# Kernel tuning notes

Hardware: AMD Instinct MI355X
Metric: run time of the kernel (lower is better)

The kernel has to match this reference:

```python
import jax, jax.numpy as jnp
import numpy as np

N = 100000      # nodes
E = 800000      # edges (avg degree 8)
F = 5           # num_node_features
D = 128         # embed_dim
H = 4           # heads
HD = D // H     # per-head dim = 32
H1, H2 = 64, 128  # mlp hidden dims


def _mlp(x, W1, b1, W2, b2, W3, b3):
    h = jax.nn.relu(x @ W1 + b1)
    h = jax.nn.relu(h @ W2 + b2)
    return h @ W3 + b3


def setup_inputs() -> dict:
    key = jax.random.key(0)
    ks = jax.random.split(key, 24)
    g = lambda i, shape: (jax.random.normal(ks[i], shape, dtype=jnp.float32) * 0.05)
    z = lambda d: jnp.zeros((d,), dtype=jnp.float32)
    return {
        "x": jax.random.normal(ks[0], (N, F), dtype=jnp.float32),
        "edge_index": jax.random.randint(ks[1], (2, E), 0, N),
        # mlp_prep: F -> 64 -> 128 -> D
        "prep_W1": g(2, (F, H1)),  "prep_b1": z(H1),
        "prep_W2": g(3, (H1, H2)), "prep_b2": z(H2),
        "prep_W3": g(4, (H2, D)),  "prep_b3": z(D),
        # mlp_update: D -> 64 -> 128 -> D
        "upd_W1": g(5, (D, H1)),   "upd_b1": z(H1),
        "upd_W2": g(6, (H1, H2)),  "upd_b2": z(H2),
        "upd_W3": g(7, (H2, D)),   "upd_b3": z(D),
        # TransformerConv projections (heads=4, per-head 32, concat -> D)
        "q_W": g(8, (D, D)),  "q_b": z(D),
        "k_W": g(9, (D, D)),  "k_b": z(D),
        "v_W": g(10, (D, D)), "v_b": z(D),
        "skip_W": g(11, (D, D)), "skip_b": z(D),
    }


def _transformer_conv(x, edge_index, q_W, q_b, k_W, k_b, v_W, v_b, skip_W, skip_b):
    # PyG TransformerConv: messages flow src=edge_index[0] -> dst=edge_index[1]
    src, dst = edge_index[0], edge_index[1]
    q = (x @ q_W + q_b).reshape(N, H, HD)
    k = (x @ k_W + k_b).reshape(N, H, HD)
    v = (x @ v_W + v_b).reshape(N, H, HD)
    scale = 1.0 / np.sqrt(HD).astype(np.float32)
    # per-edge attention logits [E, H]
    score = jnp.einsum('ehd,ehd->eh', q[dst], k[src]) * scale
    # segment softmax over incoming edges of each destination node
    m = jax.ops.segment_max(score, dst, num_segments=N)          # [N, H]
    e = jnp.exp(score - m[dst])                                  # [E, H]
    denom = jax.ops.segment_sum(e, dst, num_segments=N)         # [N, H]
    alpha = e / denom[dst]                                       # [E, H]
    # scatter-aggregate weighted values
    agg = jax.ops.segment_sum(alpha[..., None] * v[src], dst, num_segments=N)  # [N, H, HD]
    return agg.reshape(N, H * HD) + (x @ skip_W + skip_b)


def reference(x, edge_index,
              prep_W1, prep_b1, prep_W2, prep_b2, prep_W3, prep_b3,
              upd_W1, upd_b1, upd_W2, upd_b2, upd_W3, upd_b3,
              q_W, q_b, k_W, k_b, v_W, v_b, skip_W, skip_b):
    h_init = _mlp(x, prep_W1, prep_b1, prep_W2, prep_b2, prep_W3, prep_b3)
    h = _transformer_conv(h_init, edge_index, q_W, q_b, k_W, k_b, v_W, v_b, skip_W, skip_b)
    return h + _mlp(h, upd_W1, upd_b1, upd_W2, upd_b2, upd_W3, upd_b3)
```

## Files before the change

### kernel.cpp

```cpp
#include <hip/hip_runtime.h>
#include <hip/hip_bf16.h>

#define N_  100000
#define F_  5
#define D_  128
#define H_  4
#define HD_ 32
#define E_  800000

typedef __attribute__((ext_vector_type(8))) short bf16x8;
typedef __attribute__((ext_vector_type(4))) float f32x4;

__device__ __forceinline__ unsigned short f2bf(float f) {
  unsigned u = __float_as_uint(f);
  u += 0x7FFF + ((u >> 16) & 1);
  return (unsigned short)(u >> 16);
}

__device__ __forceinline__ unsigned pk2(float a, float b) {
  __hip_bfloat162 h = __float22bfloat162_rn(make_float2(a, b));
  return *(unsigned*)&h;
}

__device__ __forceinline__ float2 bf2f2(unsigned u) {
  float2 r;
  r.x = __uint_as_float(u << 16);
  r.y = __uint_as_float(u & 0xffff0000u);
  return r;
}

__device__ __forceinline__ float rowsum8(float x) {
  x += __int_as_float(__builtin_amdgcn_update_dpp(0, __float_as_int(x), 0x0B1, 0xF, 0xF, false));
  x += __int_as_float(__builtin_amdgcn_update_dpp(0, __float_as_int(x), 0x04E, 0xF, 0xF, false));
  x += __int_as_float(__builtin_amdgcn_update_dpp(0, __float_as_int(x), 0x141, 0xF, 0xF, false));
  return x;
}

template<int K, int M>
__device__ __forceinline__ void wconv_one(const float* __restrict__ W,
                                          unsigned short* __restrict__ WT,
                                          int idx) {
  const int r = idx & 7;
  const int l = (idx >> 3) & 15;
  const int rest = idx >> 7;
  const int kq = rest % (K / 8);
  const int i  = rest / (K / 8);
  WT[idx] = f2bf(W[(kq * 8 + r) * M + i * 16 + l]);
}

#define WCONV_NB 480
#define SCAN_NB ((N_ + 255) / 256)

__global__ __launch_bounds__(256) void k_wconv_all(
    const float* __restrict__ w0, const float* __restrict__ w1,
    const float* __restrict__ w2, const float* __restrict__ w3,
    const float* __restrict__ w4, const float* __restrict__ w5,
    const float* __restrict__ w6, const float* __restrict__ w7,
    const float* __restrict__ w8, unsigned short* __restrict__ WT,
    int* __restrict__ deg)
{
  if (blockIdx.x >= WCONV_NB) {
    const int i = (blockIdx.x - WCONV_NB) * 256 + threadIdx.x;
    if (i < N_) deg[i] = 0;
    return;
  }
  const int idx = blockIdx.x * 256 + threadIdx.x;
  if (idx < 8192)        wconv_one<64, 128>(w0, WT,          idx);
  else if (idx < 24576)  wconv_one<128,128>(w1, WT + 8192,   idx - 8192);
  else if (idx < 40960)  wconv_one<128,128>(w2, WT + 24576,  idx - 24576);
  else if (idx < 57344)  wconv_one<128,128>(w3, WT + 40960,  idx - 40960);
  else if (idx < 73728)  wconv_one<128,128>(w4, WT + 57344,  idx - 57344);
  else if (idx < 90112)  wconv_one<128,128>(w5, WT + 73728,  idx - 73728);
  else if (idx < 98304)  wconv_one<128, 64>(w6, WT + 90112,  idx - 90112);
  else if (idx < 106496) wconv_one<64, 128>(w7, WT + 98304,  idx - 98304);
  else                   wconv_one<128,128>(w8, WT + 106496, idx - 106496);
}

template<int K, int M>
__device__ __forceinline__ void gemm_frag(const unsigned short* sX,
                                          const unsigned short* __restrict__ WT,
                                          f32x4 (*acc)[4],
                                          int wr, int wc, int l16, int kg)
{
  constexpr int SX = K + 8;
  constexpr int IF = M / 32;
  #pragma unroll
  for (int i = 0; i < IF; ++i)
    #pragma unroll
    for (int j = 0; j < 4; ++j) acc[i][j] = (f32x4){0.f, 0.f, 0.f, 0.f};
  #pragma unroll
  for (int k0 = 0; k0 < K; k0 += 32) {
    const int kq = k0 / 8 + kg;
    bf16x8 aw[IF];
    #pragma unroll
    for (int i = 0; i < IF; ++i)
      aw[i] = *(const bf16x8*)&WT[(((wr * IF + i) * (K / 8) + kq) * 16 + l16) * 8];
    #pragma unroll
    for (int j = 0; j < 4; ++j) {
      const bf16x8 bx = *(const bf16x8*)&sX[(wc * 64 + j * 16 + l16) * SX + k0 + kg * 8];
      #pragma unroll
      for (int i = 0; i < IF; ++i)
        acc[i][j] = __builtin_amdgcn_mfma_f32_16x16x32_bf16(aw[i], bx, acc[i][j], 0, 0, 0);
    }
  }
}

template<int M, bool RELU, int SXO>
__device__ __forceinline__ void acc_to_lds(unsigned short* sY, f32x4 (*acc)[4],
                                           const float* __restrict__ bias,
                                           int wr, int wc, int l16, int kg)
{
  constexpr int IF = M / 32;
  float4 b4[IF];
  #pragma unroll
  for (int i = 0; i < IF; ++i)
    b4[i] = *(const float4*)&bias[(wr * IF + i) * 16 + kg * 4];
  #pragma unroll
  for (int j = 0; j < 4; ++j) {
    const int row = wc * 64 + j * 16 + l16;
    #pragma unroll
    for (int i = 0; i < IF; ++i) {
      const int f0 = (wr * IF + i) * 16 + kg * 4;
      float ox = acc[i][j][0] + b4[i].x, oy = acc[i][j][1] + b4[i].y;
      float oz = acc[i][j][2] + b4[i].z, ow = acc[i][j][3] + b4[i].w;
      if constexpr (RELU) {
        ox = fmaxf(ox, 0.f); oy = fmaxf(oy, 0.f);
        oz = fmaxf(oz, 0.f); ow = fmaxf(ow, 0.f);
      }
      uint2 p;
      p.x = pk2(ox, oy);
      p.y = pk2(oz, ow);
      *(uint2*)&sY[row * SXO + f0] = p;
    }
  }
}

__global__ __launch_bounds__(256) void k_prep_proj(
    const float* __restrict__ x,
    const float* __restrict__ pW1, const float* __restrict__ pb1,
    const unsigned short* __restrict__ wt_p2, const float* __restrict__ pb2,
    const unsigned short* __restrict__ wt_p3, const float* __restrict__ pb3,
    const unsigned short* __restrict__ wt_q, const float* __restrict__ qb,
    const unsigned short* __restrict__ wt_k, const float* __restrict__ kb,
    const unsigned short* __restrict__ wt_v, const float* __restrict__ vb,
    const unsigned short* __restrict__ wt_s, const float* __restrict__ sb,
    unsigned short* __restrict__ q16, unsigned short* __restrict__ k16,
    unsigned short* __restrict__ v16, float* __restrict__ out)
{
  __shared__ __align__(16) unsigned short bufA[128 * 72];
  __shared__ __align__(16) unsigned short bufB[128 * 136];

  const int t = threadIdx.x;
  const int node0 = blockIdx.x * 128;
  const int lane = t & 63;
  const int w  = t >> 6;
  const int wr = w >> 1, wc = w & 1;
  const int l16 = lane & 15, kg = lane >> 4;

  float* sxs = (float*)bufB;
  float* sw1 = (float*)bufB + 640;
  {
    const long gbase = (long)node0 * F_;
    for (int i = t; i < 128 * F_; i += 256) {
      const long g = gbase + i;
      sxs[i] = (g < (long)N_ * F_) ? x[g] : 0.f;
    }
    for (int i = t; i < 384; i += 256)
      sw1[i] = (i < 320) ? pW1[i] : pb1[i - 320];
  }
  __syncthreads();

  {
    const int n = t >> 1;
    const int half = (t & 1) * 32;
    float xr[F_];
    #pragma unroll
    for (int k = 0; k < F_; ++k) xr[k] = sxs[n * F_ + k];
    const float* sb1 = sw1 + 320;
    #pragma unroll
    for (int q = 0; q < 8; ++q) {
      float o[4];
      #pragma unroll
      for (int jj = 0; jj < 4; ++jj) {
        const int f = half + q * 4 + jj;
        float a = sb1[f];
        #pragma unroll
        for (int k = 0; k < F_; ++k) a = fmaf(xr[k], sw1[k * 64 + f], a);
        o[jj] = fmaxf(a, 0.f);
      }
      uint2 pkd;
      pkd.x = pk2(o[0], o[1]);
      pkd.y = pk2(o[2], o[3]);
      *(uint2*)&bufA[n * 72 + half + q * 4] = pkd;
    }
  }
  __syncthreads();

  f32x4 acc[4][4];

  gemm_frag<64, 128>(bufA, wt_p2, acc, wr, wc, l16, kg);
  acc_to_lds<128, true, 136>(bufB, acc, pb2, wr, wc, l16, kg);
  __syncthreads();

  gemm_frag<128, 128>(bufB, wt_p3, acc, wr, wc, l16, kg);
  __syncthreads();
  acc_to_lds<128, false, 136>(bufB, acc, pb3, wr, wc, l16, kg);
  __syncthreads();

  {
    const unsigned short* wtsP[3] = {wt_q, wt_k, wt_v};
    const float* bsP[3] = {qb, kb, vb};
    unsigned short* ysP[3] = {q16, k16, v16};
    #pragma unroll
    for (int ws = 0; ws < 3; ++ws) {
      gemm_frag<128, 128>(bufB, wtsP[ws], acc, wr, wc, l16, kg);
      const float* __restrict__ bias = bsP[ws];
      unsigned short* __restrict__ Yb = ysP[ws];
      float4 b4[4];
      #pragma unroll
      for (int i = 0; i < 4; ++i)
        b4[i] = *(const float4*)&bias[(wr * 4 + i) * 16 + kg * 4];
      #pragma unroll
      for (int j = 0; j < 4; ++j) {
        const int node = node0 + wc * 64 + j * 16 + l16;
        if (node >= N_) continue;
        #pragma unroll
        for (int i = 0; i < 4; ++i) {
          const int f0 = (wr * 4 + i) * 16 + kg * 4;
          uint2 ob;
          ob.x = pk2(acc[i][j][0] + b4[i].x, acc[i][j][1] + b4[i].y);
          ob.y = pk2(acc[i][j][2] + b4[i].z, acc[i][j][3] + b4[i].w);
          *(uint2*)&Yb[(long)node * D_ + f0] = ob;
        }
      }
    }
  }

  gemm_frag<128, 128>(bufB, wt_s, acc, wr, wc, l16, kg);
  {
    float4 b4[4];
    #pragma unroll
    for (int i = 0; i < 4; ++i)
      b4[i] = *(const float4*)&sb[(wr * 4 + i) * 16 + kg * 4];
    #pragma unroll
    for (int j = 0; j < 4; ++j) {
      const int node = node0 + wc * 64 + j * 16 + l16;
      if (node >= N_) continue;
      #pragma unroll
      for (int i = 0; i < 4; ++i) {
        const int f0 = (wr * 4 + i) * 16 + kg * 4;
        float4 o = make_float4(acc[i][j][0] + b4[i].x, acc[i][j][1] + b4[i].y,
                               acc[i][j][2] + b4[i].z, acc[i][j][3] + b4[i].w);
        *(float4*)&out[(long)node * D_ + f0] = o;
      }
    }
  }
}

__global__ __launch_bounds__(256) void k_update(
    const unsigned short* __restrict__ wt_u1, const float* __restrict__ ub1,
    const unsigned short* __restrict__ wt_u2, const float* __restrict__ ub2,
    const unsigned short* __restrict__ wt_u3, const float* __restrict__ ub3,
    float* __restrict__ out)
{
  __shared__ __align__(16) unsigned short bufA[128 * 72];
  __shared__ __align__(16) unsigned short bufB[128 * 136];

  const int t = threadIdx.x;
  const int node0 = blockIdx.x * 128;
  const int lane = t & 63;
  const int w  = t >> 6;
  const int wr = w >> 1, wc = w & 1;
  const int l16 = lane & 15, kg = lane >> 4;

  #pragma unroll
  for (int i = 0; i < 16; ++i) {
    const int g = t + 256 * i;
    const int row = g >> 5;
    const int kc  = g & 31;
    const int node = node0 + row;
    float4 xv = (node < N_) ? ((const float4*)out)[(long)node * 32 + kc]
                            : make_float4(0.f, 0.f, 0.f, 0.f);
    uint2 p;
    p.x = pk2(xv.x, xv.y);
    p.y = pk2(xv.z, xv.w);
    *(uint2*)&bufB[row * 136 + kc * 4] = p;
  }
  __syncthreads();

  f32x4 acc[4][4];

  gemm_frag<128, 64>(bufB, wt_u1, acc, wr, wc, l16, kg);
  acc_to_lds<64, true, 72>(bufA, acc, ub1, wr, wc, l16, kg);
  __syncthreads();

  gemm_frag<64, 128>(bufA, wt_u2, acc, wr, wc, l16, kg);
  acc_to_lds<128, true, 136>(bufB, acc, ub2, wr, wc, l16, kg);
  __syncthreads();

  gemm_frag<128, 128>(bufB, wt_u3, acc, wr, wc, l16, kg);
  {
    float4 b4[4];
    #pragma unroll
    for (int i = 0; i < 4; ++i)
      b4[i] = *(const float4*)&ub3[(wr * 4 + i) * 16 + kg * 4];
    #pragma unroll
    for (int j = 0; j < 4; ++j) {
      const int node = node0 + wc * 64 + j * 16 + l16;
      if (node >= N_) continue;
      #pragma unroll
      for (int i = 0; i < 4; ++i) {
        const int f0 = (wr * 4 + i) * 16 + kg * 4;
        const float4 r = *(const float4*)&out[(long)node * D_ + f0];
        float4 o = make_float4(acc[i][j][0] + b4[i].x + r.x,
                               acc[i][j][1] + b4[i].y + r.y,
                               acc[i][j][2] + b4[i].z + r.z,
                               acc[i][j][3] + b4[i].w + r.w);
        *(float4*)&out[(long)node * D_ + f0] = o;
      }
    }
  }
}

__global__ __launch_bounds__(256) void k_hist(const int* __restrict__ ei,
                                              int* __restrict__ deg) {
  int e = blockIdx.x * 256 + threadIdx.x;
  if (e < E_) atomicAdd(&deg[ei[E_ + e]], 1);
}

__global__ __launch_bounds__(256) void k_scan1(const int* __restrict__ deg,
                                               int* __restrict__ off,
                                               int* __restrict__ bsum) {
  __shared__ int s[256];
  const int t = threadIdx.x;
  const int i = blockIdx.x * 256 + t;
  const int v = (i < N_) ? deg[i] : 0;
  s[t] = v;
  __syncthreads();
  #pragma unroll
  for (int o = 1; o < 256; o <<= 1) {
    int u = (t >= o) ? s[t - o] : 0;
    __syncthreads();
    s[t] += u;
    __syncthreads();
  }
  if (i < N_) off[i] = s[t] - v;
  if (t == 255) bsum[blockIdx.x] = s[255];
}

__global__ __launch_bounds__(256) void k_scan23(const int* __restrict__ off,
                                                const int* __restrict__ bsum,
                                                int* __restrict__ cur,
                                                const int* __restrict__ deg,
                                                int2* __restrict__ meta) {
  __shared__ int sacc[256];
  const int t = threadIdx.x;
  const int bid = blockIdx.x;
  int s = 0;
  for (int j = t; j < bid; j += 256) s += bsum[j];
  sacc[t] = s;
  __syncthreads();
  #pragma unroll
  for (int o = 128; o > 0; o >>= 1) {
    if (t < o) sacc[t] += sacc[t + o];
    __syncthreads();
  }
  const int prefix = sacc[0];
  const int i = bid * 256 + t;
  if (i < N_) {
    const int o = off[i] + prefix;
    cur[i] = o;
    meta[i] = make_int2(o, deg[i]);
  }
}

__global__ __launch_bounds__(256) void k_fill(const int* __restrict__ ei,
                                              int* __restrict__ cur,
                                              int* __restrict__ esrc) {
  int e = blockIdx.x * 256 + threadIdx.x;
  if (e < E_) {
    int src = ei[e], dst = ei[E_ + e];
    int pos = atomicAdd(&cur[dst], 1);
    esrc[pos] = src;
  }
}

#define ATTN_NB 2048

__global__ __launch_bounds__(256) void k_attn(
    const int* __restrict__ esrc, const int2* __restrict__ meta,
    const unsigned short* __restrict__ q,
    const unsigned short* __restrict__ kbuf,
    const unsigned short* __restrict__ vbuf,
    float* __restrict__ out)
{
  const int lane = threadIdx.x & 63;
  const int h = lane >> 5;
  const int c = lane & 31;
  const int gwave = (blockIdx.x << 2) + (threadIdx.x >> 6);
  const int NWAVE = ATTN_NB * 4;
  const float C = 0.17677669529663687f * 1.4426950408889634f;

  for (int pair = gwave; 2 * pair < N_; pair += NWAVE) {
    const unsigned node = 2 * pair + h;
    const int2 md = meta[node];
    const int start = md.x, cnt = md.y;
    const int end = start + cnt;

    const uint2 qu = *(const uint2*)&q[(node << 7) + 4u * c];
    const float2 q01 = bf2f2(qu.x), q23 = bf2f2(qu.y);
    const float qx0 = q01.x * C, qx1 = q01.y * C;
    const float qx2 = q23.x * C, qx3 = q23.y * C;

    float l = 0.f, a0 = 0.f, a1 = 0.f, a2 = 0.f, a3 = 0.f;

    const int P = (cnt + 1) >> 1;
    if (P > 0) {
      bool v1c = (start + 1) < end;
      unsigned i0 = esrc[start];
      unsigned i1 = esrc[v1c ? start + 1 : start];
      uint2 kA = *(const uint2*)&kbuf[(i0 << 7) + 4u * c];
      uint2 kB = *(const uint2*)&kbuf[(i1 << 7) + 4u * c];
      uint2 wA = *(const uint2*)&vbuf[(i0 << 7) + 4u * c];
      uint2 wB = *(const uint2*)&vbuf[(i1 << 7) + 4u * c];
      bool v0n = (start + 2) < end, v1n = (start + 3) < end;
      unsigned i0n = esrc[v0n ? start + 2 : start];
      unsigned i1n = esrc[v1n ? start + 3 : start];

      for (int it = 0;;) {
        const bool more = (it + 1) < P;
        uint2 kAn, kBn, wAn, wBn;
        unsigned i0f = 0, i1f = 0;
        bool v0f = false, v1f = false;
        if (more) {
          kAn = *(const uint2*)&kbuf[(i0n << 7) + 4u * c];
          kBn = *(const uint2*)&kbuf[(i1n << 7) + 4u * c];
          wAn = *(const uint2*)&vbuf[(i0n << 7) + 4u * c];
          wBn = *(const uint2*)&vbuf[(i1n << 7) + 4u * c];
          const int ef = start + 2 * (it + 2);
          v0f = ef < end; v1f = (ef + 1) < end;
          i0f = esrc[v0f ? ef : start];
          i1f = esrc[v1f ? ef + 1 : start];
        }

        const float2 ka01 = bf2f2(kA.x), ka23 = bf2f2(kA.y);
        const float2 kb01 = bf2f2(kB.x), kb23 = bf2f2(kB.y);
        float sA = fmaf(qx0, ka01.x, fmaf(qx1, ka01.y, fmaf(qx2, ka23.x, qx3 * ka23.y)));
        float sB = fmaf(qx0, kb01.x, fmaf(qx1, kb01.y, fmaf(qx2, kb23.x, qx3 * kb23.y)));
        sA = rowsum8(sA);
        sB = rowsum8(sB);
        const float eA = __builtin_amdgcn_exp2f(sA);
        const float eB = v1c ? __builtin_amdgcn_exp2f(sB) : 0.f;
        const float2 va01 = bf2f2(wA.x), va23 = bf2f2(wA.y);
        const float2 vb01 = bf2f2(wB.x), vb23 = bf2f2(wB.y);
        l += eA + eB;
        a0 = fmaf(eA, va01.x, fmaf(eB, vb01.x, a0));
        a1 = fmaf(eA, va01.y, fmaf(eB, vb01.y, a1));
        a2 = fmaf(eA, va23.x, fmaf(eB, vb23.x, a2));
        a3 = fmaf(eA, va23.y, fmaf(eB, vb23.y, a3));

        if (!more) break;
        ++it;
        kA = kAn; kB = kBn; wA = wAn; wB = wBn;
        v1c = v1n;
        v0n = v0f; v1n = v1f;
        i0n = i0f; i1n = i1f;
      }
    }

    if (l > 0.f) {
      const float inv = 1.0f / l;
      float4* op = (float4*)&out[(node << 7) + 4u * c];
      float4 cv = *op;
      cv.x += a0 * inv;
      cv.y += a1 * inv;
      cv.z += a2 * inv;
      cv.w += a3 * inv;
      *op = cv;
    }
  }
}

extern "C" void kernel_launch(void* const* d_in, const int* in_sizes, int n_in,
                              void* d_out, int out_size, void* d_ws, size_t ws_size,
                              hipStream_t stream) {
  const float* x   = (const float*)d_in[0];
  const int*   ei  = (const int*)d_in[1];
  const float* pW1 = (const float*)d_in[2];  const float* pb1 = (const float*)d_in[3];
  const float* pW2 = (const float*)d_in[4];  const float* pb2 = (const float*)d_in[5];
  const float* pW3 = (const float*)d_in[6];  const float* pb3 = (const float*)d_in[7];
  const float* uW1 = (const float*)d_in[8];  const float* ub1 = (const float*)d_in[9];
  const float* uW2 = (const float*)d_in[10]; const float* ub2 = (const float*)d_in[11];
  const float* uW3 = (const float*)d_in[12]; const float* ub3 = (const float*)d_in[13];
  const float* qW  = (const float*)d_in[14]; const float* qb  = (const float*)d_in[15];
  const float* kW  = (const float*)d_in[16]; const float* kb  = (const float*)d_in[17];
  const float* vW  = (const float*)d_in[18]; const float* vb  = (const float*)d_in[19];
  const float* sW  = (const float*)d_in[20]; const float* sb  = (const float*)d_in[21];

  float* out = (float*)d_out;
  float* ws  = (float*)d_ws;

  const long ND = (long)N_ * D_;
  unsigned short* q16 = (unsigned short*)(ws + ND);
  unsigned short* k16 = (unsigned short*)(ws + 2 * ND);
  unsigned short* v16 = (unsigned short*)(ws + 3 * ND);

  unsigned short* wtb = (unsigned short*)(ws + 4 * ND);
  unsigned short* wt_p2 = wtb;
  unsigned short* wt_p3 = wtb + 8192;
  unsigned short* wt_q  = wtb + 24576;
  unsigned short* wt_k  = wtb + 40960;
  unsigned short* wt_v  = wtb + 57344;
  unsigned short* wt_s  = wtb + 73728;
  unsigned short* wt_u1 = wtb + 90112;
  unsigned short* wt_u2 = wtb + 98304;
  unsigned short* wt_u3 = wtb + 106496;

  int* deg  = (int*)ws;
  int* off  = deg + N_;
  int* cur  = off + N_;
  int* esrc = cur + N_;
  int* bsum = esrc + E_;
  int2* meta = (int2*)(bsum + 512);

  const int gT = (N_ + 127) / 128;

  k_wconv_all<<<WCONV_NB + SCAN_NB, 256, 0, stream>>>(
      pW2, pW3, qW, kW, vW, sW, uW1, uW2, uW3, wtb, deg);

  k_hist  <<<(E_ + 255) / 256, 256, 0, stream>>>(ei, deg);
  k_scan1 <<<SCAN_NB, 256, 0, stream>>>(deg, off, bsum);
  k_scan23<<<SCAN_NB, 256, 0, stream>>>(off, bsum, cur, deg, meta);
  k_fill  <<<(E_ + 255) / 256, 256, 0, stream>>>(ei, cur, esrc);

  k_prep_proj<<<gT, 256, 0, stream>>>(
      x, pW1, pb1, wt_p2, pb2, wt_p3, pb3,
      wt_q, qb, wt_k, kb, wt_v, vb, wt_s, sb,
      q16, k16, v16, out);

  k_attn<<<ATTN_NB, 256, 0, stream>>>(esrc, meta, q16, k16, v16, out);

  k_update<<<gT, 256, 0, stream>>>(wt_u1, ub1, wt_u2, ub2, wt_u3, ub3, out);
}
```

Before: 370.5 us.

## Fuse CSR build into one persistent kernel with grid barriers; flatten attention grid

Merges the histogram, two scan kernels and the fill kernel into a single 1024-block kernel separated by software global barriers on an atomic counter. This removes three kernel launches and their gaps. Separately, the attention kernel drops its grid-stride loop and launches one 32-thread group per node (N/8 blocks). The grid barrier relies on all 1024 blocks being co-resident, which risks deadlock if occupancy is lower than assumed, and the barrier spins add latency of their own.

```diff
diff --git a/kernel.cpp b/kernel.cpp
--- a/kernel.cpp
+++ b/kernel.cpp
@@ -57,11 +57,12 @@
     const float* __restrict__ w4, const float* __restrict__ w5,
     const float* __restrict__ w6, const float* __restrict__ w7,
     const float* __restrict__ w8, unsigned short* __restrict__ WT,
-    int* __restrict__ deg)
+    int* __restrict__ deg, int* __restrict__ bar)
 {
   if (blockIdx.x >= WCONV_NB) {
     const int i = (blockIdx.x - WCONV_NB) * 256 + threadIdx.x;
     if (i < N_) deg[i] = 0;
+    if (blockIdx.x == WCONV_NB && threadIdx.x < 4) bar[threadIdx.x] = 0;
     return;
   }
   const int idx = blockIdx.x * 256 + threadIdx.x;
@@ -322,70 +323,78 @@
   }
 }
 
-__global__ __launch_bounds__(256) void k_hist(const int* __restrict__ ei,
-                                              int* __restrict__ deg) {
-  int e = blockIdx.x * 256 + threadIdx.x;
-  if (e < E_) atomicAdd(&deg[ei[E_ + e]], 1);
-}
-
-__global__ __launch_bounds__(256) void k_scan1(const int* __restrict__ deg,
-                                               int* __restrict__ off,
-                                               int* __restrict__ bsum) {
+#define CSR_NB 1024
+
+__device__ __forceinline__ void gbar(int* __restrict__ bar, int phase) {
+  __syncthreads();
+  __threadfence();
+  if (threadIdx.x == 0) {
+    __hip_atomic_fetch_add(&bar[phase], 1, __ATOMIC_ACQ_REL, __HIP_MEMORY_SCOPE_AGENT);
+    while (__hip_atomic_load(&bar[phase], __ATOMIC_ACQUIRE, __HIP_MEMORY_SCOPE_AGENT) < CSR_NB)
+      __builtin_amdgcn_s_sleep(2);
+  }
+  __syncthreads();
+  __threadfence();
+}
+
+__global__ __launch_bounds__(256, 4) void k_csr(
+    const int* __restrict__ ei, int* __restrict__ deg,
+    int* __restrict__ off, int* __restrict__ bsum,
+    int* __restrict__ cur, int2* __restrict__ meta,
+    int* __restrict__ esrc, int* __restrict__ bar)
+{
   __shared__ int s[256];
   const int t = threadIdx.x;
-  const int i = blockIdx.x * 256 + t;
-  const int v = (i < N_) ? deg[i] : 0;
-  s[t] = v;
-  __syncthreads();
-  #pragma unroll
-  for (int o = 1; o < 256; o <<= 1) {
-    int u = (t >= o) ? s[t - o] : 0;
+  const int bid = blockIdx.x;
+  const int gid = bid * 256 + t;
+
+  for (int e = gid; e < E_; e += CSR_NB * 256)
+    atomicAdd(&deg[ei[E_ + e]], 1);
+  gbar(bar, 0);
+
+  if (bid < SCAN_NB) {
+    const int i = gid;
+    const int v = (i < N_) ? deg[i] : 0;
+    s[t] = v;
     __syncthreads();
-    s[t] += u;
+    #pragma unroll
+    for (int o = 1; o < 256; o <<= 1) {
+      int u = (t >= o) ? s[t - o] : 0;
+      __syncthreads();
+      s[t] += u;
+      __syncthreads();
+    }
+    if (i < N_) off[i] = s[t] - v;
+    if (t == 255) bsum[bid] = s[255];
+  }
+  gbar(bar, 1);
+
+  if (bid < SCAN_NB) {
+    int p = 0;
+    for (int j = t; j < bid; j += 256) p += bsum[j];
+    s[t] = p;
     __syncthreads();
-  }
-  if (i < N_) off[i] = s[t] - v;
-  if (t == 255) bsum[blockIdx.x] = s[255];
-}
-
-__global__ __launch_bounds__(256) void k_scan23(const int* __restrict__ off,
-                                                const int* __restrict__ bsum,
-                                                int* __restrict__ cur,
-                                                const int* __restrict__ deg,
-                                                int2* __restrict__ meta) {
-  __shared__ int sacc[256];
-  const int t = threadIdx.x;
-  const int bid = blockIdx.x;
-  int s = 0;
-  for (int j = t; j < bid; j += 256) s += bsum[j];
-  sacc[t] = s;
-  __syncthreads();
-  #pragma unroll
-  for (int o = 128; o > 0; o >>= 1) {
-    if (t < o) sacc[t] += sacc[t + o];
-    __syncthreads();
-  }
-  const int prefix = sacc[0];
-  const int i = bid * 256 + t;
-  if (i < N_) {
-    const int o = off[i] + prefix;
-    cur[i] = o;
-    meta[i] = make_int2(o, deg[i]);
-  }
-}
-
-__global__ __launch_bounds__(256) void k_fill(const int* __restrict__ ei,
-                                              int* __restrict__ cur,
-                                              int* __restrict__ esrc) {
-  int e = blockIdx.x * 256 + threadIdx.x;
-  if (e < E_) {
-    int src = ei[e], dst = ei[E_ + e];
-    int pos = atomicAdd(&cur[dst], 1);
+    #pragma unroll
+    for (int o = 128; o > 0; o >>= 1) {
+      if (t < o) s[t] += s[t + o];
+      __syncthreads();
+    }
+    const int prefix = s[0];
+    const int i = gid;
+    if (i < N_) {
+      const int o = off[i] + prefix;
+      cur[i] = o;
+      meta[i] = make_int2(o, deg[i]);
+    }
+  }
+  gbar(bar, 2);
+
+  for (int e = gid; e < E_; e += CSR_NB * 256) {
+    const int src = ei[e], dst = ei[E_ + e];
+    const int pos = atomicAdd(&cur[dst], 1);
     esrc[pos] = src;
   }
 }
-
-#define ATTN_NB 2048
 
 __global__ __launch_bounds__(256) void k_attn(
     const int* __restrict__ esrc, const int2* __restrict__ meta,
@@ -394,90 +403,85 @@
     const unsigned short* __restrict__ vbuf,
     float* __restrict__ out)
 {
-  const int lane = threadIdx.x & 63;
-  const int h = lane >> 5;
-  const int c = lane & 31;
-  const int gwave = (blockIdx.x << 2) + (threadIdx.x >> 6);
-  const int NWAVE = ATTN_NB * 4;
+  const int t = threadIdx.x;
+  const unsigned node = blockIdx.x * 8 + (t >> 5);
+  const int c = t & 31;
   const float C = 0.17677669529663687f * 1.4426950408889634f;
 
-  for (int pair = gwave; 2 * pair < N_; pair += NWAVE) {
-    const unsigned node = 2 * pair + h;
-    const int2 md = meta[node];
-    const int start = md.x, cnt = md.y;
-    const int end = start + cnt;
-
-    const uint2 qu = *(const uint2*)&q[(node << 7) + 4u * c];
-    const float2 q01 = bf2f2(qu.x), q23 = bf2f2(qu.y);
-    const float qx0 = q01.x * C, qx1 = q01.y * C;
-    const float qx2 = q23.x * C, qx3 = q23.y * C;
-
-    float l = 0.f, a0 = 0.f, a1 = 0.f, a2 = 0.f, a3 = 0.f;
-
-    const int P = (cnt + 1) >> 1;
-    if (P > 0) {
-      bool v1c = (start + 1) < end;
-      unsigned i0 = esrc[start];
-      unsigned i1 = esrc[v1c ? start + 1 : start];
-      uint2 kA = *(const uint2*)&kbuf[(i0 << 7) + 4u * c];
-      uint2 kB = *(const uint2*)&kbuf[(i1 << 7) + 4u * c];
-      uint2 wA = *(const uint2*)&vbuf[(i0 << 7) + 4u * c];
-      uint2 wB = *(const uint2*)&vbuf[(i1 << 7) + 4u * c];
-      bool v0n = (start + 2) < end, v1n = (start + 3) < end;
-      unsigned i0n = esrc[v0n ? start + 2 : start];
-      unsigned i1n = esrc[v1n ? start + 3 : start];
-
-      for (int it = 0;;) {
-        const bool more = (it + 1) < P;
-        uint2 kAn, kBn, wAn, wBn;
-        unsigned i0f = 0, i1f = 0;
-        bool v0f = false, v1f = false;
-        if (more) {
-          kAn = *(const uint2*)&kbuf[(i0n << 7) + 4u * c];
-          kBn = *(const uint2*)&kbuf[(i1n << 7) + 4u * c];
-          wAn = *(const uint2*)&vbuf[(i0n << 7) + 4u * c];
-          wBn = *(const uint2*)&vbuf[(i1n << 7) + 4u * c];
-          const int ef = start + 2 * (it + 2);
-          v0f = ef < end; v1f = (ef + 1) < end;
-          i0f = esrc[v0f ? ef : start];
-          i1f = esrc[v1f ? ef + 1 : start];
-        }
-
-        const float2 ka01 = bf2f2(kA.x), ka23 = bf2f2(kA.y);
-        const float2 kb01 = bf2f2(kB.x), kb23 = bf2f2(kB.y);
-        float sA = fmaf(qx0, ka01.x, fmaf(qx1, ka01.y, fmaf(qx2, ka23.x, qx3 * ka23.y)));
-        float sB = fmaf(qx0, kb01.x, fmaf(qx1, kb01.y, fmaf(qx2, kb23.x, qx3 * kb23.y)));
-        sA = rowsum8(sA);
-        sB = rowsum8(sB);
-        const float eA = __builtin_amdgcn_exp2f(sA);
-        const float eB = v1c ? __builtin_amdgcn_exp2f(sB) : 0.f;
-        const float2 va01 = bf2f2(wA.x), va23 = bf2f2(wA.y);
-        const float2 vb01 = bf2f2(wB.x), vb23 = bf2f2(wB.y);
-        l += eA + eB;
-        a0 = fmaf(eA, va01.x, fmaf(eB, vb01.x, a0));
-        a1 = fmaf(eA, va01.y, fmaf(eB, vb01.y, a1));
-        a2 = fmaf(eA, va23.x, fmaf(eB, vb23.x, a2));
-        a3 = fmaf(eA, va23.y, fmaf(eB, vb23.y, a3));
-
-        if (!more) break;
-        ++it;
-        kA = kAn; kB = kBn; wA = wAn; wB = wBn;
-        v1c = v1n;
-        v0n = v0f; v1n = v1f;
-        i0n = i0f; i1n = i1f;
+  const int2 md = meta[node];
+  const int start = md.x, cnt = md.y;
+  const int end = start + cnt;
+
+  const uint2 qu = *(const uint2*)&q[(node << 7) + 4u * c];
+  const float2 q01 = bf2f2(qu.x), q23 = bf2f2(qu.y);
+  const float qx0 = q01.x * C, qx1 = q01.y * C;
+  const float qx2 = q23.x * C, qx3 = q23.y * C;
+
+  float l = 0.f, a0 = 0.f, a1 = 0.f, a2 = 0.f, a3 = 0.f;
+
+  const int P = (cnt + 1) >> 1;
+  if (P > 0) {
+    bool v1c = (start + 1) < end;
+    unsigned i0 = esrc[start];
+    unsigned i1 = esrc[v1c ? start + 1 : start];
+    uint2 kA = *(const uint2*)&kbuf[(i0 << 7) + 4u * c];
+    uint2 kB = *(const uint2*)&kbuf[(i1 << 7) + 4u * c];
+    uint2 wA = *(const uint2*)&vbuf[(i0 << 7) + 4u * c];
+    uint2 wB = *(const uint2*)&vbuf[(i1 << 7) + 4u * c];
+    bool v0n = (start + 2) < end, v1n = (start + 3) < end;
+    unsigned i0n = esrc[v0n ? start + 2 : start];
+    unsigned i1n = esrc[v1n ? start + 3 : start];
+
+    for (int it = 0;;) {
+      const bool more = (it + 1) < P;
+      uint2 kAn, kBn, wAn, wBn;
+      unsigned i0f = 0, i1f = 0;
+      bool v0f = false, v1f = false;
+      if (more) {
+        kAn = *(const uint2*)&kbuf[(i0n << 7) + 4u * c];
+        kBn = *(const uint2*)&kbuf[(i1n << 7) + 4u * c];
+        wAn = *(const uint2*)&vbuf[(i0n << 7) + 4u * c];
+        wBn = *(const uint2*)&vbuf[(i1n << 7) + 4u * c];
+        const int ef = start + 2 * (it + 2);
+        v0f = ef < end; v1f = (ef + 1) < end;
+        i0f = esrc[v0f ? ef : start];
+        i1f = esrc[v1f ? ef + 1 : start];
       }
-    }
-
-    if (l > 0.f) {
-      const float inv = 1.0f / l;
-      float4* op = (float4*)&out[(node << 7) + 4u * c];
-      float4 cv = *op;
-      cv.x += a0 * inv;
-      cv.y += a1 * inv;
-      cv.z += a2 * inv;
-      cv.w += a3 * inv;
-      *op = cv;
-    }
+
+      const float2 ka01 = bf2f2(kA.x), ka23 = bf2f2(kA.y);
+      const float2 kb01 = bf2f2(kB.x), kb23 = bf2f2(kB.y);
+      float sA = fmaf(qx0, ka01.x, fmaf(qx1, ka01.y, fmaf(qx2, ka23.x, qx3 * ka23.y)));
+      float sB = fmaf(qx0, kb01.x, fmaf(qx1, kb01.y, fmaf(qx2, kb23.x, qx3 * kb23.y)));
+      sA = rowsum8(sA);
+      sB = rowsum8(sB);
+      const float eA = __builtin_amdgcn_exp2f(sA);
+      const float eB = v1c ? __builtin_amdgcn_exp2f(sB) : 0.f;
+      const float2 va01 = bf2f2(wA.x), va23 = bf2f2(wA.y);
+      const float2 vb01 = bf2f2(wB.x), vb23 = bf2f2(wB.y);
+      l += eA + eB;
+      a0 = fmaf(eA, va01.x, fmaf(eB, vb01.x, a0));
+      a1 = fmaf(eA, va01.y, fmaf(eB, vb01.y, a1));
+      a2 = fmaf(eA, va23.x, fmaf(eB, vb23.x, a2));
+      a3 = fmaf(eA, va23.y, fmaf(eB, vb23.y, a3));
+
+      if (!more) break;
+      ++it;
+      kA = kAn; kB = kBn; wA = wAn; wB = wBn;
+      v1c = v1n;
+      v0n = v0f; v1n = v1f;
+      i0n = i0f; i1n = i1f;
+    }
+  }
+
+  if (l > 0.f) {
+    const float inv = 1.0f / l;
+    float4* op = (float4*)&out[(node << 7) + 4u * c];
+    float4 cv = *op;
+    cv.x += a0 * inv;
+    cv.y += a1 * inv;
+    cv.z += a2 * inv;
+    cv.w += a3 * inv;
+    *op = cv;
   }
 }
 
@@ -522,23 +526,21 @@
   int* esrc = cur + N_;
   int* bsum = esrc + E_;
   int2* meta = (int2*)(bsum + 512);
+  int* bar  = (int*)(meta + N_);
 
   const int gT = (N_ + 127) / 128;
 
   k_wconv_all<<<WCONV_NB + SCAN_NB, 256, 0, stream>>>(
-      pW2, pW3, qW, kW, vW, sW, uW1, uW2, uW3, wtb, deg);
-
-  k_hist  <<<(E_ + 255) / 256, 256, 0, stream>>>(ei, deg);
-  k_scan1 <<<SCAN_NB, 256, 0, stream>>>(deg, off, bsum);
-  k_scan23<<<SCAN_NB, 256, 0, stream>>>(off, bsum, cur, deg, meta);
-  k_fill  <<<(E_ + 255) / 256, 256, 0, stream>>>(ei, cur, esrc);
+      pW2, pW3, qW, kW, vW, sW, uW1, uW2, uW3, wtb, deg, bar);
+
+  k_csr<<<CSR_NB, 256, 0, stream>>>(ei, deg, off, bsum, cur, meta, esrc, bar);
 
   k_prep_proj<<<gT, 256, 0, stream>>>(
       x, pW1, pb1, wt_p2, pb2, wt_p3, pb3,
       wt_q, qb, wt_k, kb, wt_v, vb, wt_s, sb,
       q16, k16, v16, out);
 
-  k_attn<<<ATTN_NB, 256, 0, stream>>>(esrc, meta, q16, k16, v16, out);
+  k_attn<<<N_ / 8, 256, 0, stream>>>(esrc, meta, q16, k16, v16, out);
 
   k_update<<<gT, 256, 0, stream>>>(wt_u1, ub1, wt_u2, ub2, wt_u3, ub3, out);
 }
```

New measurement: 857.5 us. +131.4%, slower.
